# Optimization experiments

Measured on AMD Instinct MI355X. Metric: run time of the kernel, lower is better.

The kernel has to match this reference:

```python
import jax, jax.numpy as jnp
import numpy as np

N_EMBD = 1024
N_HEAD = 16
HEAD_DIM = N_EMBD // N_HEAD
B, T = 4, 2048


def setup_inputs() -> dict:
    key = jax.random.key(0)
    ks = jax.random.split(key, 5)
    s_in = 1.0 / np.sqrt(N_EMBD)
    return {
        "x": jax.random.normal(ks[0], (B, T, N_EMBD), dtype=jnp.float32),
        "w_attn": jax.random.normal(ks[1], (N_EMBD, 3 * N_EMBD), dtype=jnp.float32) * s_in,
        "b_attn": jnp.zeros((3 * N_EMBD,), dtype=jnp.float32),
        "w_proj": jax.random.normal(ks[2], (N_EMBD, N_EMBD), dtype=jnp.float32) * s_in,
        "b_proj": jnp.zeros((N_EMBD,), dtype=jnp.float32),
    }


def reference(x, w_attn, b_attn, w_proj, b_proj):
    b, t, c = x.shape
    qkv = x @ w_attn + b_attn                      # [B,T,3C]
    q, k, v = jnp.split(qkv, 3, axis=-1)
    # [B,T,C] -> [B,H,T,D]
    def heads(z):
        return z.reshape(b, t, N_HEAD, HEAD_DIM).transpose(0, 2, 1, 3)
    q, k, v = heads(q), heads(k), heads(v)
    scale = 1.0 / np.sqrt(HEAD_DIM)
    att = jnp.einsum("bhqd,bhkd->bhqk", q, k) * scale
    causal = jnp.tril(jnp.ones((t, t), dtype=bool))
    att = jnp.where(causal, att, -jnp.inf)
    att = jax.nn.softmax(att, axis=-1)
    y = jnp.einsum("bhqk,bhkd->bhqd", att, v)      # [B,H,T,D]
    y = y.transpose(0, 2, 1, 3).reshape(b, t, c)
    return y @ w_proj + b_proj
```

## Files before the change

### kernel.cpp

```cpp
#include <hip/hip_runtime.h>
#include <hip/hip_bf16.h>

#define B_  4
#define T_  2048
#define C_  1024
#define H_  16
#define D_  64
#define C3_ 3072

typedef __attribute__((ext_vector_type(8))) short bf16x8;
typedef __attribute__((ext_vector_type(4))) float f32x4;
typedef unsigned short u16;

#define CSCALE 0.1803368801111204f

__device__ __forceinline__ u16 f2bf(float f) {
  union { float f; unsigned int u; } v; v.f = f;
  unsigned int r = (v.u + 0x7FFFu + ((v.u >> 16) & 1u)) >> 16;
  return (u16)r;
}

__device__ __forceinline__ void gload16(void* l, const void* g) {
  __builtin_amdgcn_global_load_lds(
      (const __attribute__((address_space(1))) unsigned int*)g,
      (__attribute__((address_space(3))) unsigned int*)l, 16, 0, 0);
}

__global__ __launch_bounds__(256)
void cvt_bf16(const float* __restrict__ in, u16* __restrict__ out, int n8) {
  int i = blockIdx.x * 256 + threadIdx.x;
  if (i >= n8) return;
  float4 a = *(const float4*)(in + (size_t)i * 8);
  float4 b = *(const float4*)(in + (size_t)i * 8 + 4);
  ushort4 lo, hi;
  lo.x = f2bf(a.x); lo.y = f2bf(a.y); lo.z = f2bf(a.z); lo.w = f2bf(a.w);
  hi.x = f2bf(b.x); hi.y = f2bf(b.y); hi.z = f2bf(b.z); hi.w = f2bf(b.w);
  *(ushort4*)(out + (size_t)i * 8) = lo;
  *(ushort4*)(out + (size_t)i * 8 + 4) = hi;
}

__global__ __launch_bounds__(256)
void transcvt2(const float* __restrict__ wa, u16* __restrict__ waT,
               const float* __restrict__ wp, u16* __restrict__ wpT) {
  const int bx = blockIdx.x;
  const float* w; u16* wT; int N, n;
  if (bx < 48) { w = wa; wT = waT; N = C3_; n = bx * 64 + (threadIdx.x & 63); }
  else         { w = wp; wT = wpT; N = C_;  n = (bx - 48) * 64 + (threadIdx.x & 63); }
  const int k0 = blockIdx.y * 16 + (threadIdx.x >> 6) * 4;
  float v0 = w[(size_t)(k0 + 0) * N + n];
  float v1 = w[(size_t)(k0 + 1) * N + n];
  float v2 = w[(size_t)(k0 + 2) * N + n];
  float v3 = w[(size_t)(k0 + 3) * N + n];
  ushort4 o; o.x = f2bf(v0); o.y = f2bf(v1); o.z = f2bf(v2); o.w = f2bf(v3);
  *(ushort4*)(wT + (size_t)n * 1024 + k0) = o;
}

template <typename OutT, int BM, bool VSPLIT>
__global__ __launch_bounds__(512, 2)
void gemm256(const u16* __restrict__ A, const u16* __restrict__ Bt,
             const float* __restrict__ bias, OutT* __restrict__ C,
             u16* __restrict__ vTout, int M, int N, int K, int qscale_cols) {
  constexpr int AG = BM * 8;
  constexpr int S  = AG + 2048;
  constexpr int MF = BM / 64;
  constexpr int ALOADS = BM / 128;
  __shared__ int4 lds[2 * S];

  const int tid = threadIdx.x, lane = tid & 63, wid = tid >> 6;
  const int wr = wid >> 2, wc = wid & 3;
  const int row0 = blockIdx.y * BM, col0 = blockIdx.x * 256;

  f32x4 acc[2 * MF][4];
#pragma unroll
  for (int m = 0; m < 2 * MF; ++m)
#pragma unroll
    for (int nf = 0; nf < 4; ++nf) acc[m][nf] = (f32x4){0.f, 0.f, 0.f, 0.f};

  const u16* pA[2][ALOADS]; const u16* pB[2][2];
#pragma unroll
  for (int h = 0; h < 2; ++h) {
#pragma unroll
    for (int i = 0; i < ALOADS; ++i) {
      int g = h * (AG / 2) + i * 512 + tid;
      int rr = ((g >> 7) << 4) + (g & 15), ko = ((g >> 4) & 7) * 8;
      pA[h][i] = A + (size_t)(row0 + rr) * K + ko;
    }
#pragma unroll
    for (int i = 0; i < 2; ++i) {
      int g = h * 1024 + i * 512 + tid;
      int rr = ((g >> 7) << 4) + (g & 15), ko = ((g >> 4) & 7) * 8;
      pB[h][i] = Bt + (size_t)(col0 + rr) * K + ko;
    }
  }

  auto stage = [&](int t, int isA, int h, int buf) {
    if (isA) {
      int4* d = &lds[buf * S + h * (AG / 2) + wid * 64];
      gload16(d, pA[h][0] + t * 64);
      if constexpr (ALOADS == 2) gload16(d + 512, pA[h][1] + t * 64);
    } else {
      int4* d = &lds[buf * S + AG + h * 1024 + wid * 64];
      gload16(d, pB[h][0] + t * 64);
      gload16(d + 512, pB[h][1] + t * 64);
    }
  };
  auto rdA = [&](int f, int kk, int buf) {
    return *(const bf16x8*)&lds[buf * S + (wr * (2 * MF) + f) * 128 + kk * 64 + lane];
  };
  auto rdB = [&](int nf, int kk, int buf) {
    return *(const bf16x8*)&lds[buf * S + AG + (wc * 4 + nf) * 128 + kk * 64 + lane];
  };

#define WAIT_KEEP() do { if constexpr (BM == 256) \
    asm volatile("s_waitcnt vmcnt(6)" ::: "memory"); else \
    asm volatile("s_waitcnt vmcnt(5)" ::: "memory"); } while (0)

  const int nk = K >> 6, nit = nk >> 1;

  stage(0, 1, 0, 0); stage(0, 1, 1, 0); stage(0, 0, 0, 0); stage(0, 0, 1, 0);
  stage(1, 0, 0, 1); stage(1, 0, 1, 1); stage(1, 1, 0, 1);
  WAIT_KEEP();
  __builtin_amdgcn_s_barrier();

  for (int it = 0; it < nit; ++it) {
    const int t1g = 2 * it + 1, t2g = t1g + 1, t3g = t1g + 2;
    bf16x8 a0[MF][2], a1[MF][2], b0[2][2], b1[2][2];

#pragma unroll
    for (int m = 0; m < MF; ++m) { a0[m][0] = rdA(m, 0, 0); a0[m][1] = rdA(m, 1, 0); }
#pragma unroll
    for (int nf = 0; nf < 2; ++nf) { b0[nf][0] = rdB(nf, 0, 0); b0[nf][1] = rdB(nf, 1, 0); }
    stage(t1g, 1, 1, 1);
    __builtin_amdgcn_s_barrier();
    __builtin_amdgcn_s_setprio(1);
#pragma unroll
    for (int m = 0; m < MF; ++m)
#pragma unroll
      for (int nf = 0; nf < 2; ++nf) {
        acc[m][nf] = __builtin_amdgcn_mfma_f32_16x16x32_bf16(a0[m][0], b0[nf][0], acc[m][nf], 0, 0, 0);
        acc[m][nf] = __builtin_amdgcn_mfma_f32_16x16x32_bf16(a0[m][1], b0[nf][1], acc[m][nf], 0, 0, 0);
      }
    __builtin_amdgcn_s_setprio(0);
    __builtin_amdgcn_s_barrier();

#pragma unroll
    for (int nf = 0; nf < 2; ++nf) { b1[nf][0] = rdB(2 + nf, 0, 0); b1[nf][1] = rdB(2 + nf, 1, 0); }
    __builtin_amdgcn_s_barrier();
    __builtin_amdgcn_s_setprio(1);
#pragma unroll
    for (int m = 0; m < MF; ++m)
#pragma unroll
      for (int nf = 0; nf < 2; ++nf) {
        acc[m][2 + nf] = __builtin_amdgcn_mfma_f32_16x16x32_bf16(a0[m][0], b1[nf][0], acc[m][2 + nf], 0, 0, 0);
        acc[m][2 + nf] = __builtin_amdgcn_mfma_f32_16x16x32_bf16(a0[m][1], b1[nf][1], acc[m][2 + nf], 0, 0, 0);
      }
    __builtin_amdgcn_s_setprio(0);
    __builtin_amdgcn_s_barrier();

#pragma unroll
    for (int m = 0; m < MF; ++m) { a1[m][0] = rdA(MF + m, 0, 0); a1[m][1] = rdA(MF + m, 1, 0); }
    if (t2g < nk) stage(t2g, 0, 0, 0);
    __builtin_amdgcn_s_barrier();
    __builtin_amdgcn_s_setprio(1);
#pragma unroll
    for (int m = 0; m < MF; ++m)
#pragma unroll
      for (int nf = 0; nf < 2; ++nf) {
        acc[MF + m][2 + nf] = __builtin_amdgcn_mfma_f32_16x16x32_bf16(a1[m][0], b1[nf][0], acc[MF + m][2 + nf], 0, 0, 0);
        acc[MF + m][2 + nf] = __builtin_amdgcn_mfma_f32_16x16x32_bf16(a1[m][1], b1[nf][1], acc[MF + m][2 + nf], 0, 0, 0);
      }
    __builtin_amdgcn_s_setprio(0);
    __builtin_amdgcn_s_barrier();

    if (t2g < nk) {
      stage(t2g, 0, 1, 0);
      stage(t2g, 1, 0, 0);
      WAIT_KEEP();
    } else {
      asm volatile("s_waitcnt vmcnt(0)" ::: "memory");
    }
    __builtin_amdgcn_s_barrier();
    __builtin_amdgcn_s_setprio(1);
#pragma unroll
    for (int m = 0; m < MF; ++m)
#pragma unroll
      for (int nf = 0; nf < 2; ++nf) {
        acc[MF + m][nf] = __builtin_amdgcn_mfma_f32_16x16x32_bf16(a1[m][0], b0[nf][0], acc[MF + m][nf], 0, 0, 0);
        acc[MF + m][nf] = __builtin_amdgcn_mfma_f32_16x16x32_bf16(a1[m][1], b0[nf][1], acc[MF + m][nf], 0, 0, 0);
      }
    __builtin_amdgcn_s_setprio(0);
    __builtin_amdgcn_s_barrier();

#pragma unroll
    for (int m = 0; m < MF; ++m) { a0[m][0] = rdA(m, 0, 1); a0[m][1] = rdA(m, 1, 1); }
#pragma unroll
    for (int nf = 0; nf < 2; ++nf) { b0[nf][0] = rdB(nf, 0, 1); b0[nf][1] = rdB(nf, 1, 1); }
    if (t2g < nk) stage(t2g, 1, 1, 0);
    __builtin_amdgcn_s_barrier();
    __builtin_amdgcn_s_setprio(1);
#pragma unroll
    for (int m = 0; m < MF; ++m)
#pragma unroll
      for (int nf = 0; nf < 2; ++nf) {
        acc[m][nf] = __builtin_amdgcn_mfma_f32_16x16x32_bf16(a0[m][0], b0[nf][0], acc[m][nf], 0, 0, 0);
        acc[m][nf] = __builtin_amdgcn_mfma_f32_16x16x32_bf16(a0[m][1], b0[nf][1], acc[m][nf], 0, 0, 0);
      }
    __builtin_amdgcn_s_setprio(0);
    __builtin_amdgcn_s_barrier();

#pragma unroll
    for (int nf = 0; nf < 2; ++nf) { b1[nf][0] = rdB(2 + nf, 0, 1); b1[nf][1] = rdB(2 + nf, 1, 1); }
    __builtin_amdgcn_s_barrier();
    __builtin_amdgcn_s_setprio(1);
#pragma unroll
    for (int m = 0; m < MF; ++m)
#pragma unroll
      for (int nf = 0; nf < 2; ++nf) {
        acc[m][2 + nf] = __builtin_amdgcn_mfma_f32_16x16x32_bf16(a0[m][0], b1[nf][0], acc[m][2 + nf], 0, 0, 0);
        acc[m][2 + nf] = __builtin_amdgcn_mfma_f32_16x16x32_bf16(a0[m][1], b1[nf][1], acc[m][2 + nf], 0, 0, 0);
      }
    __builtin_amdgcn_s_setprio(0);
    __builtin_amdgcn_s_barrier();

#pragma unroll
    for (int m = 0; m < MF; ++m) { a1[m][0] = rdA(MF + m, 0, 1); a1[m][1] = rdA(MF + m, 1, 1); }
    if (t3g < nk) stage(t3g, 0, 0, 1);
    __builtin_amdgcn_s_barrier();
    __builtin_amdgcn_s_setprio(1);
#pragma unroll
    for (int m = 0; m < MF; ++m)
#pragma unroll
      for (int nf = 0; nf < 2; ++nf) {
        acc[MF + m][2 + nf] = __builtin_amdgcn_mfma_f32_16x16x32_bf16(a1[m][0], b1[nf][0], acc[MF + m][2 + nf], 0, 0, 0);
        acc[MF + m][2 + nf] = __builtin_amdgcn_mfma_f32_16x16x32_bf16(a1[m][1], b1[nf][1], acc[MF + m][2 + nf], 0, 0, 0);
      }
    __builtin_amdgcn_s_setprio(0);
    __builtin_amdgcn_s_barrier();

    if (t3g < nk) {
      stage(t3g, 0, 1, 1);
      stage(t3g, 1, 0, 1);
      WAIT_KEEP();
    } else {
      asm volatile("s_waitcnt vmcnt(0)" ::: "memory");
    }
    __builtin_amdgcn_s_barrier();
    __builtin_amdgcn_s_setprio(1);
#pragma unroll
    for (int m = 0; m < MF; ++m)
#pragma unroll
      for (int nf = 0; nf < 2; ++nf) {
        acc[MF + m][nf] = __builtin_amdgcn_mfma_f32_16x16x32_bf16(a1[m][0], b0[nf][0], acc[MF + m][nf], 0, 0, 0);
        acc[MF + m][nf] = __builtin_amdgcn_mfma_f32_16x16x32_bf16(a1[m][1], b0[nf][1], acc[MF + m][nf], 0, 0, 0);
      }
    __builtin_amdgcn_s_setprio(0);
    __builtin_amdgcn_s_barrier();
  }
#undef WAIT_KEEP

  const int cc = lane & 15, qg = lane >> 4;
#pragma unroll
  for (int m = 0; m < 2 * MF; ++m) {
#pragma unroll
    for (int nf = 0; nf < 4; ++nf) {
      const int gc = col0 + wc * 64 + nf * 16 + cc;
      const float bv = bias[gc];
      const int gr0 = row0 + wr * (BM / 2) + m * 16 + qg * 4;
      if (VSPLIT && gc >= 2 * C_) {
        const int hh = (gc - 2 * C_) >> 6, d = (gc - 2 * C_) & 63;
        const int bb = gr0 >> 11, tloc = gr0 & 2047;
        ushort4 pk;
        pk.x = f2bf(acc[m][nf][0] + bv);
        pk.y = f2bf(acc[m][nf][1] + bv);
        pk.z = f2bf(acc[m][nf][2] + bv);
        pk.w = f2bf(acc[m][nf][3] + bv);
        *(ushort4*)(vTout + ((size_t)(bb * 16 + hh) * 64 + d) * T_ + tloc) = pk;
      } else {
        const float sc = (gc < qscale_cols) ? CSCALE : 1.0f;
#pragma unroll
        for (int r = 0; r < 4; ++r) {
          float val = (acc[m][nf][r] + bv) * sc;
          if constexpr (sizeof(OutT) == 2)
            ((u16*)C)[(size_t)(gr0 + r) * N + gc] = f2bf(val);
          else
            ((float*)C)[(size_t)(gr0 + r) * N + gc] = val;
        }
      }
    }
  }
}

__global__ __launch_bounds__(512, 4)
void attn_mfma(const u16* __restrict__ qkv, const u16* __restrict__ vT,
               u16* __restrict__ yout) {
  __shared__ int4 Ks4[512];
  __shared__ int4 Vs4[512];
  __shared__ int4 Ps4[2048];

  const int n   = blockIdx.x;
  const int xcd = n & 7, t = n >> 3;
  const int bh  = xcd * 8 + (t >> 3);
  const int ip  = t & 7;
  const int b   = bh >> 4, h = bh & 15;

  const int tid = threadIdx.x;
  const int lane = tid & 63, wq = tid >> 6;
  const int sub = wq & 3;
  const int cc = lane & 15, qg = lane >> 4;

  const int qt128 = (wq < 4) ? ip : (15 - ip);
  const int qrow0 = qt128 * 128 + sub * 32;
  const int diag  = qt128 * 2 + (sub >> 1);
  const int jn    = 32 - 2 * ip;

  const u16* kbase = qkv + (size_t)b * T_ * C3_ + C_ + h * D_;
  const u16* vtb   = vT + (size_t)bh * D_ * T_;

  bf16x8 qf[2][2];
#pragma unroll
  for (int hf = 0; hf < 2; ++hf) {
    const u16* qb = qkv + (size_t)(b * T_ + qrow0 + hf * 16 + cc) * C3_ + h * D_;
    qf[hf][0] = *(const bf16x8*)(qb + qg * 8);
    qf[hf][1] = *(const bf16x8*)(qb + 32 + qg * 8);
  }

  const u16* kg = kbase + (size_t)((tid >> 7) * 16 + (tid & 15)) * C3_ +
                  ((tid >> 6) & 1) * 32 + ((tid >> 4) & 3) * 8;
  const u16* vg = vtb + (size_t)((tid >> 7) * 16 + (tid & 15)) * T_ +
                  ((tid >> 6) & 1) * 32 + ((tid >> 4) & 3) * 8;

  int4 kpref = *(const int4*)kg;
  int4 vpref = *(const int4*)vg;

  float m_r[2] = {-1e30f, -1e30f}, l_r[2] = {0.f, 0.f};
  f32x4 o[2][4];
#pragma unroll
  for (int hf = 0; hf < 2; ++hf)
#pragma unroll
    for (int db = 0; db < 4; ++db) o[hf][db] = (f32x4){0.f, 0.f, 0.f, 0.f};

  for (int j = 0; j < jn; ++j) {
    __syncthreads();
    Ks4[tid] = kpref;
    Vs4[tid] = vpref;
    __syncthreads();
    if (j + 1 < jn) {
      kpref = *(const int4*)(kg + (size_t)(j + 1) * 64 * C3_);
      vpref = *(const int4*)(vg + (j + 1) * 64);
    }
    if (j > diag) continue;

    __builtin_amdgcn_s_setprio(1);
    f32x4 s[2][4];
#pragma unroll
    for (int kb = 0; kb < 4; ++kb) {
      bf16x8 kf0 = *(const bf16x8*)(Ks4 + kb * 128 + lane);
      bf16x8 kf1 = *(const bf16x8*)(Ks4 + kb * 128 + 64 + lane);
#pragma unroll
      for (int hf = 0; hf < 2; ++hf) {
        f32x4 z = (f32x4){0.f, 0.f, 0.f, 0.f};
        z = __builtin_amdgcn_mfma_f32_16x16x32_bf16(kf0, qf[hf][0], z, 0, 0, 0);
        z = __builtin_amdgcn_mfma_f32_16x16x32_bf16(kf1, qf[hf][1], z, 0, 0, 0);
        s[hf][kb] = z;
      }
    }
    __builtin_amdgcn_s_setprio(0);

    if (j == diag) {
#pragma unroll
      for (int hf = 0; hf < 2; ++hf) {
        const int qabs = qrow0 + hf * 16 + cc;
#pragma unroll
        for (int kb = 0; kb < 4; ++kb)
#pragma unroll
          for (int r = 0; r < 4; ++r)
            if ((j * 64 + kb * 16 + qg * 4 + r) > qabs) s[hf][kb][r] = -1e30f;
      }
    }

#pragma unroll
    for (int hf = 0; hf < 2; ++hf) {
      float mx = s[hf][0][0];
#pragma unroll
      for (int kb = 0; kb < 4; ++kb)
#pragma unroll
        for (int r = 0; r < 4; ++r) mx = fmaxf(mx, s[hf][kb][r]);
      mx = fmaxf(mx, __shfl_xor(mx, 16));
      mx = fmaxf(mx, __shfl_xor(mx, 32));

      if (!__all(mx <= m_r[hf])) {
        float mn = fmaxf(m_r[hf], mx);
        float al = exp2f(m_r[hf] - mn);
        m_r[hf] = mn;
        l_r[hf] *= al;
        float alq[4];
#pragma unroll
        for (int r = 0; r < 4; ++r)
          alq[r] = __shfl(al, (lane & 48) | (qg * 4 + r));
#pragma unroll
        for (int db = 0; db < 4; ++db)
#pragma unroll
          for (int r = 0; r < 4; ++r) o[hf][db][r] *= alq[r];
      }

      float lsum = 0.f;
#pragma unroll
      for (int kb = 0; kb < 4; ++kb)
#pragma unroll
        for (int r = 0; r < 4; ++r) {
          float p = exp2f(s[hf][kb][r] - m_r[hf]);
          s[hf][kb][r] = p;
          lsum += p;
        }
      l_r[hf] += lsum;

      char* myPb = (char*)(Ps4 + wq * 256 + hf * 128);
#pragma unroll
      for (int kb = 0; kb < 4; ++kb) {
        unsigned plo, phi;
        asm("v_cvt_pk_bf16_f32 %0, %1, %2" : "=v"(plo) : "v"(s[hf][kb][0]), "v"(s[hf][kb][1]));
        asm("v_cvt_pk_bf16_f32 %0, %1, %2" : "=v"(phi) : "v"(s[hf][kb][2]), "v"(s[hf][kb][3]));
        const int kv0 = kb * 16 + qg * 4;
        const int g = ((kv0 >> 5) << 6) + (((kv0 >> 3) & 3) << 4) + cc;
        uint2 pk; pk.x = plo; pk.y = phi;
        *(uint2*)(myPb + g * 16 + (kv0 & 7) * 2) = pk;
      }
    }

    bf16x8 pa[2][2];
#pragma unroll
    for (int hf = 0; hf < 2; ++hf)
#pragma unroll
      for (int ks = 0; ks < 2; ++ks)
        pa[hf][ks] = *(const bf16x8*)(Ps4 + wq * 256 + hf * 128 + ks * 64 + lane);
    __builtin_amdgcn_s_setprio(1);
#pragma unroll
    for (int db = 0; db < 4; ++db) {
#pragma unroll
      for (int ks = 0; ks < 2; ++ks) {
        bf16x8 vf = *(const bf16x8*)(Vs4 + db * 128 + ks * 64 + lane);
        o[0][db] = __builtin_amdgcn_mfma_f32_16x16x32_bf16(pa[0][ks], vf, o[0][db], 0, 0, 0);
        o[1][db] = __builtin_amdgcn_mfma_f32_16x16x32_bf16(pa[1][ks], vf, o[1][db], 0, 0, 0);
      }
    }
    __builtin_amdgcn_s_setprio(0);
  }

#pragma unroll
  for (int hf = 0; hf < 2; ++hf) {
    float ls = l_r[hf];
    ls += __shfl_xor(ls, 16);
    ls += __shfl_xor(ls, 32);
    float linv_l = 1.0f / ls;
    float linv[4];
#pragma unroll
    for (int r = 0; r < 4; ++r)
      linv[r] = __shfl(linv_l, (lane & 48) | (qg * 4 + r));

    u16* yb = yout + (size_t)(b * T_ + qrow0 + hf * 16 + qg * 4) * C_ + h * D_ + cc;
#pragma unroll
    for (int db = 0; db < 4; ++db)
#pragma unroll
      for (int r = 0; r < 4; ++r)
        yb[(size_t)r * C_ + db * 16] = f2bf(o[hf][db][r] * linv[r]);
  }
}

extern "C" void kernel_launch(void* const* d_in, const int* in_sizes, int n_in,
                              void* d_out, int out_size, void* d_ws, size_t ws_size,
                              hipStream_t stream) {
  const float* x      = (const float*)d_in[0];
  const float* w_attn = (const float*)d_in[1];
  const float* b_attn = (const float*)d_in[2];
  const float* w_proj = (const float*)d_in[3];
  const float* b_proj = (const float*)d_in[4];
  float* out = (float*)d_out;

  char* ws = (char*)d_ws;
  u16* xb  = (u16*)(ws);
  u16* waT = (u16*)(ws + 16777216);
  u16* wpT = (u16*)(ws + 23068672);
  u16* qkv = (u16*)(ws + 25165824);
  u16* yb  = (u16*)(ws + 75497472);
  u16* vT  = (u16*)(ws + 92274688);

  cvt_bf16<<<4096, 256, 0, stream>>>(x, xb, (B_ * T_ * C_) / 8);
  transcvt2<<<dim3(64, 64), 256, 0, stream>>>(w_attn, waT, w_proj, wpT);

  gemm256<u16, 256, true><<<dim3(C3_ / 256, (B_ * T_) / 256), 512, 0, stream>>>(
      xb, waT, b_attn, qkv, vT, B_ * T_, C3_, C_, C_);

  attn_mfma<<<dim3(8 * H_ * B_), 512, 0, stream>>>(qkv, vT, yb);

  gemm256<float, 128, false><<<dim3(C_ / 256, (B_ * T_) / 128), 512, 0, stream>>>(
      yb, wpT, b_proj, out, nullptr, B_ * T_, C_, C_, 0);
}
```

Baseline: 211.8 us.

## Double attention KV tile to 128 rows and merge prep conversion kernels

The attention kernel now stages 128 keys/values per loop iteration instead of 64, so it runs half as many block-wide barrier pairs and global prefetch rounds. Each staged tile is then processed as two 64-wide sub-steps with the same online softmax. LDS use grows, which may lower occupancy below the requested 4 blocks per CU, and waves on earlier diagonals sit idle through more of each larger tile. Separately, the x conversion and the weight transpose-conversion are fused into one launch to remove a kernel launch.

Measured after the change: 257.3 us. 21.5% more time.

```diff
diff --git a/kernel.cpp b/kernel.cpp
--- a/kernel.cpp
+++ b/kernel.cpp
@@ -27,32 +27,34 @@
 }
 
 __global__ __launch_bounds__(256)
-void cvt_bf16(const float* __restrict__ in, u16* __restrict__ out, int n8) {
-  int i = blockIdx.x * 256 + threadIdx.x;
-  if (i >= n8) return;
-  float4 a = *(const float4*)(in + (size_t)i * 8);
-  float4 b = *(const float4*)(in + (size_t)i * 8 + 4);
-  ushort4 lo, hi;
-  lo.x = f2bf(a.x); lo.y = f2bf(a.y); lo.z = f2bf(a.z); lo.w = f2bf(a.w);
-  hi.x = f2bf(b.x); hi.y = f2bf(b.y); hi.z = f2bf(b.z); hi.w = f2bf(b.w);
-  *(ushort4*)(out + (size_t)i * 8) = lo;
-  *(ushort4*)(out + (size_t)i * 8 + 4) = hi;
-}
-
-__global__ __launch_bounds__(256)
-void transcvt2(const float* __restrict__ wa, u16* __restrict__ waT,
-               const float* __restrict__ wp, u16* __restrict__ wpT) {
-  const int bx = blockIdx.x;
-  const float* w; u16* wT; int N, n;
-  if (bx < 48) { w = wa; wT = waT; N = C3_; n = bx * 64 + (threadIdx.x & 63); }
-  else         { w = wp; wT = wpT; N = C_;  n = (bx - 48) * 64 + (threadIdx.x & 63); }
-  const int k0 = blockIdx.y * 16 + (threadIdx.x >> 6) * 4;
-  float v0 = w[(size_t)(k0 + 0) * N + n];
-  float v1 = w[(size_t)(k0 + 1) * N + n];
-  float v2 = w[(size_t)(k0 + 2) * N + n];
-  float v3 = w[(size_t)(k0 + 3) * N + n];
-  ushort4 o; o.x = f2bf(v0); o.y = f2bf(v1); o.z = f2bf(v2); o.w = f2bf(v3);
-  *(ushort4*)(wT + (size_t)n * 1024 + k0) = o;
+void prep(const float* __restrict__ x, u16* __restrict__ xb,
+          const float* __restrict__ wa, u16* __restrict__ waT,
+          const float* __restrict__ wp, u16* __restrict__ wpT) {
+  const int bid = blockIdx.x;
+  const int tid = threadIdx.x;
+  if (bid < 4096) {
+    const int i = bid * 256 + tid;
+    float4 a = *(const float4*)(x + (size_t)i * 8);
+    float4 b = *(const float4*)(x + (size_t)i * 8 + 4);
+    ushort4 lo, hi;
+    lo.x = f2bf(a.x); lo.y = f2bf(a.y); lo.z = f2bf(a.z); lo.w = f2bf(a.w);
+    hi.x = f2bf(b.x); hi.y = f2bf(b.y); hi.z = f2bf(b.z); hi.w = f2bf(b.w);
+    *(ushort4*)(xb + (size_t)i * 8) = lo;
+    *(ushort4*)(xb + (size_t)i * 8 + 4) = hi;
+  } else {
+    const int b2 = bid - 4096;
+    const int bx = b2 & 63, by = b2 >> 6;
+    const float* w; u16* wT; int N, n;
+    if (bx < 48) { w = wa; wT = waT; N = C3_; n = bx * 64 + (tid & 63); }
+    else         { w = wp; wT = wpT; N = C_;  n = (bx - 48) * 64 + (tid & 63); }
+    const int k0 = by * 16 + (tid >> 6) * 4;
+    float v0 = w[(size_t)(k0 + 0) * N + n];
+    float v1 = w[(size_t)(k0 + 1) * N + n];
+    float v2 = w[(size_t)(k0 + 2) * N + n];
+    float v3 = w[(size_t)(k0 + 3) * N + n];
+    ushort4 o; o.x = f2bf(v0); o.y = f2bf(v1); o.z = f2bf(v2); o.w = f2bf(v3);
+    *(ushort4*)(wT + (size_t)n * 1024 + k0) = o;
+  }
 }
 
 template <typename OutT, int BM, bool VSPLIT>
@@ -293,8 +295,8 @@
 __global__ __launch_bounds__(512, 4)
 void attn_mfma(const u16* __restrict__ qkv, const u16* __restrict__ vT,
                u16* __restrict__ yout) {
-  __shared__ int4 Ks4[512];
-  __shared__ int4 Vs4[512];
+  __shared__ int4 Ks4[1024];
+  __shared__ int4 Vs4[1024];
   __shared__ int4 Ps4[2048];
 
   const int n   = blockIdx.x;
@@ -310,8 +312,8 @@
 
   const int qt128 = (wq < 4) ? ip : (15 - ip);
   const int qrow0 = qt128 * 128 + sub * 32;
-  const int diag  = qt128 * 2 + (sub >> 1);
-  const int jn    = 32 - 2 * ip;
+  const int d64   = qt128 * 2 + (sub >> 1);
+  const int jn    = 16 - ip;
 
   const u16* kbase = qkv + (size_t)b * T_ * C3_ + C_ + h * D_;
   const u16* vtb   = vT + (size_t)bh * D_ * T_;
@@ -324,13 +326,18 @@
     qf[hf][1] = *(const bf16x8*)(qb + 32 + qg * 8);
   }
 
-  const u16* kg = kbase + (size_t)((tid >> 7) * 16 + (tid & 15)) * C3_ +
-                  ((tid >> 6) & 1) * 32 + ((tid >> 4) & 3) * 8;
-  const u16* vg = vtb + (size_t)((tid >> 7) * 16 + (tid & 15)) * T_ +
-                  ((tid >> 6) & 1) * 32 + ((tid >> 4) & 3) * 8;
-
-  int4 kpref = *(const int4*)kg;
-  int4 vpref = *(const int4*)vg;
+  const int g1 = tid, g2 = tid + 512;
+  const u16* kgA = kbase + (size_t)((g1 >> 7) * 16 + (g1 & 15)) * C3_ +
+                   ((g1 >> 6) & 1) * 32 + ((g1 >> 4) & 3) * 8;
+  const u16* kgB = kbase + (size_t)((g2 >> 7) * 16 + (g2 & 15)) * C3_ +
+                   ((g2 >> 6) & 1) * 32 + ((g2 >> 4) & 3) * 8;
+  const u16* vgA = vtb + (size_t)((g1 >> 8) * 16 + (g1 & 15)) * T_ +
+                   ((g1 >> 4) & 15) * 8;
+  const u16* vgB = vtb + (size_t)((g2 >> 8) * 16 + (g2 & 15)) * T_ +
+                   ((g2 >> 4) & 15) * 8;
+
+  int4 k0p = *(const int4*)kgA, k1p = *(const int4*)kgB;
+  int4 v0p = *(const int4*)vgA, v1p = *(const int4*)vgB;
 
   float m_r[2] = {-1e30f, -1e30f}, l_r[2] = {0.f, 0.f};
   f32x4 o[2][4];
@@ -341,109 +348,118 @@
 
   for (int j = 0; j < jn; ++j) {
     __syncthreads();
-    Ks4[tid] = kpref;
-    Vs4[tid] = vpref;
+    Ks4[g1] = k0p; Ks4[g2] = k1p;
+    Vs4[g1] = v0p; Vs4[g2] = v1p;
     __syncthreads();
     if (j + 1 < jn) {
-      kpref = *(const int4*)(kg + (size_t)(j + 1) * 64 * C3_);
-      vpref = *(const int4*)(vg + (j + 1) * 64);
-    }
-    if (j > diag) continue;
-
-    __builtin_amdgcn_s_setprio(1);
-    f32x4 s[2][4];
-#pragma unroll
-    for (int kb = 0; kb < 4; ++kb) {
-      bf16x8 kf0 = *(const bf16x8*)(Ks4 + kb * 128 + lane);
-      bf16x8 kf1 = *(const bf16x8*)(Ks4 + kb * 128 + 64 + lane);
+      const size_t ko = (size_t)(j + 1) * 128 * C3_;
+      k0p = *(const int4*)(kgA + ko); k1p = *(const int4*)(kgB + ko);
+      v0p = *(const int4*)(vgA + (j + 1) * 128);
+      v1p = *(const int4*)(vgB + (j + 1) * 128);
+    }
+    if (j > qt128) continue;
+
+#pragma unroll
+    for (int hs = 0; hs < 2; ++hs) {
+      const int s64 = 2 * j + hs;
+      if (s64 > d64) continue;
+
+      __builtin_amdgcn_s_setprio(1);
+      f32x4 s[2][4];
+#pragma unroll
+      for (int kb = 0; kb < 4; ++kb) {
+        bf16x8 kf0 = *(const bf16x8*)(Ks4 + (hs * 4 + kb) * 128 + lane);
+        bf16x8 kf1 = *(const bf16x8*)(Ks4 + (hs * 4 + kb) * 128 + 64 + lane);
+#pragma unroll
+        for (int hf = 0; hf < 2; ++hf) {
+          f32x4 z = (f32x4){0.f, 0.f, 0.f, 0.f};
+          z = __builtin_amdgcn_mfma_f32_16x16x32_bf16(kf0, qf[hf][0], z, 0, 0, 0);
+          z = __builtin_amdgcn_mfma_f32_16x16x32_bf16(kf1, qf[hf][1], z, 0, 0, 0);
+          s[hf][kb] = z;
+        }
+      }
+      __builtin_amdgcn_s_setprio(0);
+
+      if (s64 == d64) {
+#pragma unroll
+        for (int hf = 0; hf < 2; ++hf) {
+          const int qabs = qrow0 + hf * 16 + cc;
+#pragma unroll
+          for (int kb = 0; kb < 4; ++kb)
+#pragma unroll
+            for (int r = 0; r < 4; ++r)
+              if ((j * 128 + hs * 64 + kb * 16 + qg * 4 + r) > qabs)
+                s[hf][kb][r] = -1e30f;
+        }
+      }
+
 #pragma unroll
       for (int hf = 0; hf < 2; ++hf) {
-        f32x4 z = (f32x4){0.f, 0.f, 0.f, 0.f};
-        z = __builtin_amdgcn_mfma_f32_16x16x32_bf16(kf0, qf[hf][0], z, 0, 0, 0);
-        z = __builtin_amdgcn_mfma_f32_16x16x32_bf16(kf1, qf[hf][1], z, 0, 0, 0);
-        s[hf][kb] = z;
-      }
-    }
-    __builtin_amdgcn_s_setprio(0);
-
-    if (j == diag) {
-#pragma unroll
-      for (int hf = 0; hf < 2; ++hf) {
-        const int qabs = qrow0 + hf * 16 + cc;
+        float mx = s[hf][0][0];
 #pragma unroll
         for (int kb = 0; kb < 4; ++kb)
 #pragma unroll
+          for (int r = 0; r < 4; ++r) mx = fmaxf(mx, s[hf][kb][r]);
+        mx = fmaxf(mx, __shfl_xor(mx, 16));
+        mx = fmaxf(mx, __shfl_xor(mx, 32));
+
+        if (!__all(mx <= m_r[hf])) {
+          float mn = fmaxf(m_r[hf], mx);
+          float al = exp2f(m_r[hf] - mn);
+          m_r[hf] = mn;
+          l_r[hf] *= al;
+          float alq[4];
+#pragma unroll
           for (int r = 0; r < 4; ++r)
-            if ((j * 64 + kb * 16 + qg * 4 + r) > qabs) s[hf][kb][r] = -1e30f;
-      }
-    }
-
-#pragma unroll
-    for (int hf = 0; hf < 2; ++hf) {
-      float mx = s[hf][0][0];
-#pragma unroll
-      for (int kb = 0; kb < 4; ++kb)
-#pragma unroll
-        for (int r = 0; r < 4; ++r) mx = fmaxf(mx, s[hf][kb][r]);
-      mx = fmaxf(mx, __shfl_xor(mx, 16));
-      mx = fmaxf(mx, __shfl_xor(mx, 32));
-
-      if (!__all(mx <= m_r[hf])) {
-        float mn = fmaxf(m_r[hf], mx);
-        float al = exp2f(m_r[hf] - mn);
-        m_r[hf] = mn;
-        l_r[hf] *= al;
-        float alq[4];
-#pragma unroll
-        for (int r = 0; r < 4; ++r)
-          alq[r] = __shfl(al, (lane & 48) | (qg * 4 + r));
-#pragma unroll
-        for (int db = 0; db < 4; ++db)
-#pragma unroll
-          for (int r = 0; r < 4; ++r) o[hf][db][r] *= alq[r];
-      }
-
-      float lsum = 0.f;
-#pragma unroll
-      for (int kb = 0; kb < 4; ++kb)
-#pragma unroll
-        for (int r = 0; r < 4; ++r) {
-          float p = exp2f(s[hf][kb][r] - m_r[hf]);
-          s[hf][kb][r] = p;
-          lsum += p;
+            alq[r] = __shfl(al, (lane & 48) | (qg * 4 + r));
+#pragma unroll
+          for (int db = 0; db < 4; ++db)
+#pragma unroll
+            for (int r = 0; r < 4; ++r) o[hf][db][r] *= alq[r];
         }
-      l_r[hf] += lsum;
-
-      char* myPb = (char*)(Ps4 + wq * 256 + hf * 128);
-#pragma unroll
-      for (int kb = 0; kb < 4; ++kb) {
-        unsigned plo, phi;
-        asm("v_cvt_pk_bf16_f32 %0, %1, %2" : "=v"(plo) : "v"(s[hf][kb][0]), "v"(s[hf][kb][1]));
-        asm("v_cvt_pk_bf16_f32 %0, %1, %2" : "=v"(phi) : "v"(s[hf][kb][2]), "v"(s[hf][kb][3]));
-        const int kv0 = kb * 16 + qg * 4;
-        const int g = ((kv0 >> 5) << 6) + (((kv0 >> 3) & 3) << 4) + cc;
-        uint2 pk; pk.x = plo; pk.y = phi;
-        *(uint2*)(myPb + g * 16 + (kv0 & 7) * 2) = pk;
-      }
-    }
-
-    bf16x8 pa[2][2];
-#pragma unroll
-    for (int hf = 0; hf < 2; ++hf)
-#pragma unroll
-      for (int ks = 0; ks < 2; ++ks)
-        pa[hf][ks] = *(const bf16x8*)(Ps4 + wq * 256 + hf * 128 + ks * 64 + lane);
-    __builtin_amdgcn_s_setprio(1);
-#pragma unroll
-    for (int db = 0; db < 4; ++db) {
-#pragma unroll
-      for (int ks = 0; ks < 2; ++ks) {
-        bf16x8 vf = *(const bf16x8*)(Vs4 + db * 128 + ks * 64 + lane);
-        o[0][db] = __builtin_amdgcn_mfma_f32_16x16x32_bf16(pa[0][ks], vf, o[0][db], 0, 0, 0);
-        o[1][db] = __builtin_amdgcn_mfma_f32_16x16x32_bf16(pa[1][ks], vf, o[1][db], 0, 0, 0);
-      }
-    }
-    __builtin_amdgcn_s_setprio(0);
+
+        float lsum = 0.f;
+#pragma unroll
+        for (int kb = 0; kb < 4; ++kb)
+#pragma unroll
+          for (int r = 0; r < 4; ++r) {
+            float p = exp2f(s[hf][kb][r] - m_r[hf]);
+            s[hf][kb][r] = p;
+            lsum += p;
+          }
+        l_r[hf] += lsum;
+
+        char* myPb = (char*)(Ps4 + wq * 256 + hf * 128);
+#pragma unroll
+        for (int kb = 0; kb < 4; ++kb) {
+          unsigned plo, phi;
+          asm("v_cvt_pk_bf16_f32 %0, %1, %2" : "=v"(plo) : "v"(s[hf][kb][0]), "v"(s[hf][kb][1]));
+          asm("v_cvt_pk_bf16_f32 %0, %1, %2" : "=v"(phi) : "v"(s[hf][kb][2]), "v"(s[hf][kb][3]));
+          const int kv0 = kb * 16 + qg * 4;
+          const int g = ((kv0 >> 5) << 6) + (((kv0 >> 3) & 3) << 4) + cc;
+          uint2 pk; pk.x = plo; pk.y = phi;
+          *(uint2*)(myPb + g * 16 + (kv0 & 7) * 2) = pk;
+        }
+      }
+
+      bf16x8 pa[2][2];
+#pragma unroll
+      for (int hf = 0; hf < 2; ++hf)
+#pragma unroll
+        for (int ks = 0; ks < 2; ++ks)
+          pa[hf][ks] = *(const bf16x8*)(Ps4 + wq * 256 + hf * 128 + ks * 64 + lane);
+      __builtin_amdgcn_s_setprio(1);
+#pragma unroll
+      for (int db = 0; db < 4; ++db) {
+#pragma unroll
+        for (int ks = 0; ks < 2; ++ks) {
+          bf16x8 vf = *(const bf16x8*)(Vs4 + db * 256 + (hs * 2 + ks) * 64 + lane);
+          o[0][db] = __builtin_amdgcn_mfma_f32_16x16x32_bf16(pa[0][ks], vf, o[0][db], 0, 0, 0);
+          o[1][db] = __builtin_amdgcn_mfma_f32_16x16x32_bf16(pa[1][ks], vf, o[1][db], 0, 0, 0);
+        }
+      }
+      __builtin_amdgcn_s_setprio(0);
+    }
   }
 
 #pragma unroll
@@ -484,8 +500,7 @@
   u16* yb  = (u16*)(ws + 75497472);
   u16* vT  = (u16*)(ws + 92274688);
 
-  cvt_bf16<<<4096, 256, 0, stream>>>(x, xb, (B_ * T_ * C_) / 8);
-  transcvt2<<<dim3(64, 64), 256, 0, stream>>>(w_attn, waT, w_proj, wpT);
+  prep<<<8192, 256, 0, stream>>>(x, xb, w_attn, waT, w_proj, wpT);
 
   gemm256<u16, 256, true><<<dim3(C3_ / 256, (B_ * T_) / 256), 512, 0, stream>>>(
       xb, waT, b_attn, qkv, vT, B_ * T_, C3_, C_, C_);
```
